# Kernel optimization log

Hardware: AMD Instinct MI355X
Metric: run time of the kernel (lower is better)

## Reference

```python
import jax, jax.numpy as jnp
import numpy as np

ALPHA = 0.05   # propalpha
GDEP = 2       # gcn_depth
DIL = 2        # new_dilation
KSET = (2, 3, 6, 7)

def _dconv(x, w, b, d):
    # Conv2d(c_in, c_out, (1, k), dilation=(1, d), padding='same'), NCHW layout
    k = w.shape[-1]
    tot = d * (k - 1)
    lo = tot // 2
    y = jax.lax.conv_general_dilated(x, w, (1, 1), ((0, 0), (lo, tot - lo)),
                                     rhs_dilation=(1, d),
                                     dimension_numbers=('NCHW', 'OIHW', 'NCHW'))
    return y + b[None, :, None, None]

def _inception(x, ws, bs):
    # 'same' padding keeps seq_len for every branch, so the tail-slice is a no-op
    return jnp.concatenate([_dconv(x, w, b, DIL) for w, b in zip(ws, bs)], axis=1)

def _gcn(Hf, Aoff, W, b, n):
    # PyG GCNConv with unit edge weights (no edge_weight passed) and remaining self-loops:
    # out = D^-1/2 (A_off + I_R)^T D^-1/2 (Hf @ W^T) + b, where only rows < n carry edges.
    XW = Hf @ W.T
    deg = jnp.ones((Hf.shape[0],), Hf.dtype).at[:n].add(jnp.sum(Aoff, axis=0))
    dis = jax.lax.rsqrt(deg)
    out = XW / deg[:, None]                                           # self-loop term
    out = out.at[:n].add(dis[:n, None] * (Aoff.T @ (dis[:n, None] * XW[:n])))
    return out + b[None, :]

def _mixprop(X, A, gws, gbs, mw, mb):
    B, C, n, L = X.shape
    # dense_to_sparse ignores weights here (none passed to GCNConv) -> binary adjacency;
    # add_remaining_self_loops replaces any diagonal entries, so zero the diagonal.
    Aoff = (A != 0).astype(X.dtype) * (1.0 - jnp.eye(n, dtype=X.dtype))
    H = X
    hops = [X]
    for i in range(GDEP):
        Hf = H.reshape(B * L, C * n)   # torch row-major reshape, replicated exactly
        H1 = _gcn(Hf, Aoff, gws[i], gbs[i], n)
        H = ALPHA * X + H1.reshape(B, C, n, L)
        hops.append(H)
    Hc = jnp.concatenate(hops, axis=1)  # (B, (GDEP+1)*C, n, L)
    return jnp.einsum('bixl,oi->boxl', Hc, mw) + mb[None, :, None, None]

def _layernorm(x, w, b, idx, eps=1e-5):
    # F.layer_norm over all of x.shape[1:] with node-indexed affine params
    mu = jnp.mean(x, axis=(1, 2, 3), keepdims=True)
    var = jnp.var(x, axis=(1, 2, 3), keepdims=True)
    xh = (x - mu) * jax.lax.rsqrt(var + eps)
    return xh * w[:, idx, :][None] + b[:, idx, :][None]

def _forward(x, x_skip, A, idx, fws, fbs, gws, gbs, skip_w, skip_b,
             mp1_gw, mp1_gb, mp1_mw, mp1_mb, mp2_gw, mp2_gb, mp2_mw, mp2_mb,
             ln_w, ln_b):
    x_res = x
    xf = jnp.tanh(_inception(x, fws, fbs))
    xg = jax.nn.sigmoid(_inception(x, gws, gbs))
    x = xf * xg  # gated dilated temporal conv (dropout is an eval-mode no-op)
    x_skip = jnp.einsum('bixl,oi->boxl', x, skip_w) + skip_b[None, :, None, None] + x_skip
    x = (_mixprop(x, A, mp1_gw, mp1_gb, mp1_mw, mp1_mb)
         + _mixprop(x.swapaxes(0, 0), A.T, mp2_gw, mp2_gb, mp2_mw, mp2_mb))
    x = x + x_res[..., -x.shape[3]:]
    x = _layernorm(x, ln_w, ln_b, idx)
    return x, x_skip

def setup_inputs():
    key = jax.random.key(0)
    ks = jax.random.split(key, 32)
    B, C, N, L, SKIP = 16, 32, 128, 128, 64
    F = C * N
    co = C // len(KSET)
    d = {}
    d['x'] = jax.random.normal(ks[0], (B, C, N, L), jnp.float32)
    d['x_skip'] = jax.random.normal(ks[1], (B, SKIP, N, L), jnp.float32)
    d['A'] = jax.random.uniform(ks[2], (N, N), jnp.float32)
    d['idx'] = jnp.arange(N, dtype=jnp.int32)
    i = 3
    for pre in ('f', 'g'):
        for k in KSET:
            d[pre + 'w' + str(k)] = jax.random.normal(ks[i], (co, C, 1, k), jnp.float32) * float(1.0 / np.sqrt(C * k))
            d[pre + 'b' + str(k)] = jax.random.uniform(ks[i + 1], (co,), jnp.float32)
            i += 2
    d['skip_w'] = jax.random.normal(ks[i], (SKIP, C), jnp.float32) * float(1.0 / np.sqrt(C)); i += 1
    d['skip_b'] = jax.random.uniform(ks[i], (SKIP,), jnp.float32); i += 1
    for mp in ('mp1', 'mp2'):
        d[mp + '_gw'] = jax.random.normal(ks[i], (GDEP, F, F), jnp.float32) * float(1.0 / np.sqrt(F)); i += 1
        d[mp + '_gb'] = jnp.zeros((GDEP, F), jnp.float32)
        d[mp + '_mw'] = jax.random.normal(ks[i], (C, (GDEP + 1) * C), jnp.float32) * float(1.0 / np.sqrt((GDEP + 1) * C)); i += 1
        d[mp + '_mb'] = jax.random.uniform(ks[i], (C,), jnp.float32); i += 1
    d['ln_w'] = jnp.ones((C, N, L), jnp.float32)
    d['ln_b'] = jnp.zeros((C, N, L), jnp.float32)
    return d

def reference(x, x_skip, A, idx, fw2, fb2, fw3, fb3, fw6, fb6, fw7, fb7,
              gw2, gb2, gw3, gb3, gw6, gb6, gw7, gb7, skip_w, skip_b,
              mp1_gw, mp1_gb, mp1_mw, mp1_mb, mp2_gw, mp2_gb, mp2_mw, mp2_mb,
              ln_w, ln_b):
    return _forward(x, x_skip, A, idx,
                    [fw2, fw3, fw6, fw7], [fb2, fb3, fb6, fb7],
                    [gw2, gw3, gw6, gw7], [gb2, gb3, gb6, gb7],
                    skip_w, skip_b, mp1_gw, mp1_gb, mp1_mw, mp1_mb,
                    mp2_gw, mp2_gb, mp2_mw, mp2_mb, ln_w, ln_b)
```

## Files before the change

### kernel.cpp

```cpp
#include <hip/hip_runtime.h>
#include <stdint.h>

typedef unsigned short u16;
typedef unsigned int   u32;
typedef __attribute__((ext_vector_type(4))) float f32x4;
typedef __attribute__((ext_vector_type(8))) short bf16x8;

__device__ __forceinline__ u16 f2bf(float f) {
    u32 i = __float_as_uint(f);
    u32 r = (i + 0x7fffu + ((i >> 16) & 1u)) >> 16;
    return (u16)r;
}
__device__ __forceinline__ float bf2f(u16 u) {
    return __uint_as_float(((u32)u) << 16);
}
__device__ __forceinline__ u32 cvt2bf(float a, float b) {
    u32 r;
    asm("v_cvt_pk_bf16_f32 %0, %1, %2" : "=v"(r) : "v"(a), "v"(b));
    return r;
}

#define GLOAD16(g, l) __builtin_amdgcn_global_load_lds( \
    (const __attribute__((address_space(1))) void*)(g), \
    (__attribute__((address_space(3))) void*)(l), 16, 0, 0)

__global__ void k_prep(const float* __restrict__ A, float* dis1, float* inv1,
                       float* dis2, float* inv2)
{
    int r = threadIdx.x;
    if (r >= 128) return;
    int cc = 0, cr = 0;
    for (int j = 0; j < 128; ++j) {
        if (j == r) continue;
        if (A[(j << 7) + r] != 0.f) cc++;
        if (A[(r << 7) + j] != 0.f) cr++;
    }
    float d1 = 1.f + (float)cc, d2 = 1.f + (float)cr;
    dis1[r] = rsqrtf(d1); inv1[r] = 1.f / d1;
    dis2[r] = rsqrtf(d2); inv2[r] = 1.f / d2;
}

__global__ __launch_bounds__(256)
void k_wcvt2(const float* __restrict__ W0, const float* __restrict__ W1,
             u16* __restrict__ Wb0, u16* __restrict__ Wb1)
{
    int half = blockIdx.x >> 13;
    const float* W = half ? W1 : W0;
    u16* Wb = half ? Wb1 : Wb0;
    size_t e = ((size_t)(blockIdx.x & 8191) * 256 + threadIdx.x) * 8;
    f32x4 a = *(const f32x4*)(W + e);
    f32x4 b = *(const f32x4*)(W + e + 4);
    uint4 r;
    r.x = cvt2bf(a[0], a[1]); r.y = cvt2bf(a[2], a[3]);
    r.z = cvt2bf(b[0], b[1]); r.w = cvt2bf(b[2], b[3]);
    *(uint4*)(Wb + e) = r;
}

__global__ __launch_bounds__(256, 2)
void k_gemm2g(const u16* __restrict__ A0, const u16* __restrict__ A1,
              const u16* __restrict__ B0, const u16* __restrict__ B1,
              const u16* __restrict__ Gres,
              const float* __restrict__ gb0, const float* __restrict__ gb1,
              u16* __restrict__ Ha, u16* __restrict__ Hb,
              float* __restrict__ XW0a, float* __restrict__ XW0b)
{
    __shared__ alignas(16) u16 As[128 * 32];
    __shared__ alignas(16) u16 Bs[128 * 32];
    const int K = 4096;
    const int tid  = threadIdx.x;
    const int lane = tid & 63;
    const int w    = tid >> 6;

    int bid = (blockIdx.z * gridDim.y + blockIdx.y) * gridDim.x + blockIdx.x;
    int swz = (bid & 7) * 128 + (bid >> 3);
    int z   = swz >> 9;
    int rem = swz & 511;
    const int bm = (rem >> 5) * 128, bn = (rem & 31) * 128;
    const int wm = (w >> 1) * 64,    wn = (w & 1) * 64;

    const u16* A = z ? A1 : A0;
    const u16* B = z ? B1 : B0;

    const int srow = tid >> 2, scol = (tid & 3) * 8;
    const u16* ag = A + (size_t)(bm + srow) * K + scol;
    const u16* bg = B + (size_t)(bn + srow) * K + scol;
    u16* asl = As + tid * 8;
    u16* bsl = Bs + tid * 8;
    const size_t rstep = (size_t)64 * K;

    f32x4 acc[4][4] = {};
    const int lr = lane & 15, lkb = (lane >> 4) * 8;

    for (int k0 = 0; k0 < K; k0 += 32) {
        GLOAD16(ag + k0,         asl);
        GLOAD16(ag + k0 + rstep, asl + 2048);
        GLOAD16(bg + k0,         bsl);
        GLOAD16(bg + k0 + rstep, bsl + 2048);
        __syncthreads();
        bf16x8 af[4], bfv[4];
        #pragma unroll
        for (int i = 0; i < 4; ++i) {
            af[i]  = *(const bf16x8*)(As + (wm + i * 16 + lr) * 32 + lkb);
            bfv[i] = *(const bf16x8*)(Bs + (wn + i * 16 + lr) * 32 + lkb);
        }
        #pragma unroll
        for (int i = 0; i < 4; ++i)
            #pragma unroll
            for (int j = 0; j < 4; ++j)
                acc[i][j] = __builtin_amdgcn_mfma_f32_16x16x32_bf16(af[i], bfv[j], acc[i][j], 0, 0, 0);
        __syncthreads();
    }

    const int orow = (lane >> 4) * 4, ocol = lane & 15;
    const float* gbv = z ? gb1 : gb0;
    u16* H = z ? Hb : Ha;

    #pragma unroll
    for (int j = 0; j < 4; ++j) {
        const int o = bn + wn + j * 16 + ocol;
        const float gbo = gbv[o];
        #pragma unroll
        for (int i = 0; i < 4; ++i) {
            const int rbase = bm + wm + i * 16 + orow;
            #pragma unroll
            for (int v = 0; v < 4; ++v) {
                const size_t e = (size_t)(rbase + v) * 4096 + o;
                float g = bf2f(Gres[e]);
                H[e] = f2bf(__fmaf_rn(0.05f, g, acc[i][j][v] + gbo));
            }
        }
    }
    if (bm == 0) {
        float* XW0 = z ? XW0b : XW0a;
        #pragma unroll
        for (int i = 0; i < 4; ++i) {
            #pragma unroll
            for (int j = 0; j < 4; ++j) {
                float* cp = XW0 + (size_t)(wm + i * 16 + orow) * 4096 + (bn + wn + j * 16 + ocol);
                #pragma unroll
                for (int v = 0; v < 4; ++v)
                    cp[(size_t)v * 4096] = acc[i][j][v];
            }
        }
    }
}

__global__ __launch_bounds__(256)
void k_gcnfix(const float* __restrict__ XW0a, const float* __restrict__ XW0b,
              const u16* __restrict__ G, const float* __restrict__ Af,
              const float* __restrict__ dis1, const float* __restrict__ inv1,
              const float* __restrict__ dis2, const float* __restrict__ inv2,
              const float* __restrict__ gb0, const float* __restrict__ gb1,
              u16* __restrict__ Ha, u16* __restrict__ Hb)
{
    const int prob = blockIdx.x >> 9;
    const int rem  = blockIdx.x & 511;
    const int t4 = rem * 256 + threadIdx.x;
    const int r = t4 >> 10, og = (t4 & 1023) << 2;
    const float* XW0 = prob ? XW0b : XW0a;
    const float* dis = prob ? dis2 : dis1;
    const float* inv = prob ? inv2 : inv1;
    const float* gb  = prob ? gb1  : gb0;
    u16* H = prob ? Hb : Ha;

    const size_t e = ((size_t)r << 12) + og;
    f32x4 xw = *(const f32x4*)(XW0 + e);
    f32x4 s = {0.f, 0.f, 0.f, 0.f};
    for (int j = 0; j < 128; ++j) {
        float av = prob ? Af[(r << 7) + j] : Af[(j << 7) + r];
        float wv = ((av != 0.f) && (j != r)) ? dis[j] : 0.f;
        f32x4 xv = *(const f32x4*)(XW0 + ((size_t)j << 12) + og);
        #pragma unroll
        for (int q = 0; q < 4; ++q) s[q] = __fmaf_rn(wv, xv[q], s[q]);
    }
    const float iv = inv[r], dr = dis[r];
    f32x4 gb4 = *(const f32x4*)(gb + og);
    uint2 gv = *(const uint2*)(G + e);
    float g0 = __uint_as_float(gv.x << 16), g1 = __uint_as_float(gv.x & 0xffff0000u);
    float g2 = __uint_as_float(gv.y << 16), g3 = __uint_as_float(gv.y & 0xffff0000u);
    float y0 = __fmaf_rn(0.05f, g0, __fmaf_rn(dr, s[0], xw[0] * iv) + gb4[0]);
    float y1 = __fmaf_rn(0.05f, g1, __fmaf_rn(dr, s[1], xw[1] * iv) + gb4[1]);
    float y2 = __fmaf_rn(0.05f, g2, __fmaf_rn(dr, s[2], xw[2] * iv) + gb4[2]);
    float y3 = __fmaf_rn(0.05f, g3, __fmaf_rn(dr, s[3], xw[3] * iv) + gb4[3]);
    uint2 rr;
    rr.x = cvt2bf(y0, y1);
    rr.y = cvt2bf(y2, y3);
    *(uint2*)(H + e) = rr;
}

__device__ __forceinline__ constexpr int wbase_of(int k) {
    return k == 2 ? 0 : k == 3 ? 520 : k == 6 ? 1296 : 2840;
}
__device__ __forceinline__ constexpr int ob_of(int k) {
    return k == 2 ? 0 : k == 3 ? 8 : k == 6 ? 16 : 24;
}

template<int K_>
__device__ __forceinline__ void conv_phase(const float* __restrict__ xsb,
                                           const float* __restrict__ wfp,
                                           const float* __restrict__ wgp,
                                           float fb, float gb,
                                           u16* __restrict__ Gp)
{
    float accf[8], accg[8];
    #pragma unroll
    for (int i = 0; i < 8; ++i) { accf[i] = fb; accg[i] = gb; }
    for (int c = 0; c < 32; ++c) {
        float xw[24];
        const float* xr = xsb + c * 144;
        #pragma unroll
        for (int q = 0; q < 6; ++q) {
            f32x4 v = *(const f32x4*)(xr + q * 4);
            xw[q * 4 + 0] = v[0]; xw[q * 4 + 1] = v[1];
            xw[q * 4 + 2] = v[2]; xw[q * 4 + 3] = v[3];
        }
        float wfj[K_], wgj[K_];
        const float* wfc = wfp + c * K_;
        const float* wgc = wgp + c * K_;
        #pragma unroll
        for (int j = 0; j < K_; ++j) { wfj[j] = wfc[j]; wgj[j] = wgc[j]; }
        #pragma unroll
        for (int li = 0; li < 8; ++li) {
            #pragma unroll
            for (int j = 0; j < K_; ++j) {
                float xv = xw[li + 8 - (K_ - 1) + 2 * j];
                accf[li] = __fmaf_rn(xv, wfj[j], accf[li]);
                accg[li] = __fmaf_rn(xv, wgj[j], accg[li]);
            }
        }
    }
    u16 o8[8];
    #pragma unroll
    for (int i = 0; i < 8; ++i) {
        float e2 = __expf(2.f * accf[i]);
        float th = 1.f - __fdividef(2.f, e2 + 1.f);
        float sg = __fdividef(1.f, 1.f + __expf(-accg[i]));
        o8[i] = f2bf(th * sg);
    }
    uint4 u;
    u.x = o8[0] | ((u32)o8[1] << 16); u.y = o8[2] | ((u32)o8[3] << 16);
    u.z = o8[4] | ((u32)o8[5] << 16); u.w = o8[6] | ((u32)o8[7] << 16);
    *(uint4*)Gp = u;
}

template<int KA, int KB>
__device__ __forceinline__ void wave_pair(const float* __restrict__ xs,
                                          const float* __restrict__ wfl,
                                          const float* __restrict__ wgl,
                                          const float* __restrict__ fbl,
                                          const float* __restrict__ gbl,
                                          int oo, int lL, int b, int n,
                                          u16* __restrict__ G)
{
    {
        constexpr int BS = wbase_of(KA), ST = 32 * KA + 1, OB = ob_of(KA);
        const int o = OB + oo, l0 = lL * 8;
        conv_phase<KA>(xs + l0, wfl + BS + oo * ST, wgl + BS + oo * ST,
                       fbl[o], gbl[o],
                       G + (((size_t)(b * 32 + o) * 128 + n) * 128 + l0));
    }
    {
        constexpr int BS = wbase_of(KB), ST = 32 * KB + 1, OB = ob_of(KB);
        const int o = OB + oo, l0 = 64 + lL * 8;
        conv_phase<KB>(xs + l0, wfl + BS + oo * ST, wgl + BS + oo * ST,
                       fbl[o], gbl[o],
                       G + (((size_t)(b * 32 + o) * 128 + n) * 128 + l0));
    }
}

__global__ __launch_bounds__(256)
void k_incep(const float* __restrict__ x,
             const float* __restrict__ fw2p, const float* __restrict__ fw3p,
             const float* __restrict__ fw6p, const float* __restrict__ fw7p,
             const float* __restrict__ fb2p, const float* __restrict__ fb3p,
             const float* __restrict__ fb6p, const float* __restrict__ fb7p,
             const float* __restrict__ gw2p, const float* __restrict__ gw3p,
             const float* __restrict__ gw6p, const float* __restrict__ gw7p,
             const float* __restrict__ gb2p, const float* __restrict__ gb3p,
             const float* __restrict__ gb6p, const float* __restrict__ gb7p,
             u16* __restrict__ G)
{
    __shared__ alignas(16) float xs[32 * 144];
    __shared__ float wfl[4640], wgl[4640];
    __shared__ float fbl[32], gbl[32];
    const int tid = threadIdx.x;
    const int b = blockIdx.x >> 7, n = blockIdx.x & 127;

    for (int i = tid; i < 32 * 144; i += 256) xs[i] = 0.f;
    for (int g = tid; g < 4608; g += 256) {
        int rel, k, woff;
        const float *pf, *pg;
        if (g < 512)       { rel = g;        k = 2; woff = 0;    pf = fw2p; pg = gw2p; }
        else if (g < 1280) { rel = g - 512;  k = 3; woff = 520;  pf = fw3p; pg = gw3p; }
        else if (g < 2816) { rel = g - 1280; k = 6; woff = 1296; pf = fw6p; pg = gw6p; }
        else               { rel = g - 2816; k = 7; woff = 2840; pf = fw7p; pg = gw7p; }
        int ck = 32 * k;
        int oo = rel / ck, rem = rel % ck;
        int dst = woff + oo * (ck + 1) + rem;
        wfl[dst] = pf[rel];
        wgl[dst] = pg[rel];
    }
    if (tid < 32) {
        int br = tid >> 3, oo = tid & 7;
        const float* pf = br == 0 ? fb2p : br == 1 ? fb3p : br == 2 ? fb6p : fb7p;
        const float* pg = br == 0 ? gb2p : br == 1 ? gb3p : br == 2 ? gb6p : gb7p;
        fbl[tid] = pf[oo]; gbl[tid] = pg[oo];
    }
    __syncthreads();
    const float* xb = x + (size_t)b * 524288 + n * 128;
    for (int p = 0; p < 4; ++p) {
        int chunk = p * 256 + tid;
        int c = chunk >> 5, l4 = (chunk & 31) * 4;
        *(f32x4*)&xs[c * 144 + 8 + l4] = *(const f32x4*)(xb + (size_t)c * 16384 + l4);
    }
    __syncthreads();

    const int w = tid >> 6, lane = tid & 63;
    const int oo = lane >> 3, lL = lane & 7;
    switch (w) {
        case 0:  wave_pair<2, 7>(xs, wfl, wgl, fbl, gbl, oo, lL, b, n, G); break;
        case 1:  wave_pair<7, 2>(xs, wfl, wgl, fbl, gbl, oo, lL, b, n, G); break;
        case 2:  wave_pair<3, 6>(xs, wfl, wgl, fbl, gbl, oo, lL, b, n, G); break;
        default: wave_pair<6, 3>(xs, wfl, wgl, fbl, gbl, oo, lL, b, n, G); break;
    }
}

__global__ __launch_bounds__(256)
void k_skip(const u16* __restrict__ G, const float* __restrict__ xskip,
            const float* __restrict__ sw, const float* __restrict__ sb,
            float* __restrict__ outp)
{
    __shared__ alignas(16) u16 Gs[4096];
    __shared__ float swl[64 * 33];
    __shared__ float sbl[64];
    const int tid = threadIdx.x;
    const int b = blockIdx.x >> 7, n = blockIdx.x & 127;
    const u16* gb_ = G + (size_t)b * 524288 + n * 128;
    for (int p = 0; p < 2; ++p) {
        int chunk = p * 256 + tid, c = chunk >> 4, l8 = (chunk & 15) * 8;
        *(uint4*)&Gs[c * 128 + l8] = *(const uint4*)(gb_ + (size_t)c * 16384 + l8);
    }
    for (int i = tid; i < 2048; i += 256) swl[(i >> 5) * 33 + (i & 31)] = sw[i];
    if (tid < 64) sbl[tid] = sb[tid];
    __syncthreads();
    const int sg = (tid & 15) * 4, l0 = (tid >> 4) * 8;
    float acc[4][8];
    #pragma unroll
    for (int si = 0; si < 4; ++si) {
        float bv = sbl[sg + si];
        #pragma unroll
        for (int li = 0; li < 8; ++li) acc[si][li] = bv;
    }
    for (int c = 0; c < 32; ++c) {
        uint4 gv = *(const uint4*)&Gs[c * 128 + l0];
        float g[8];
        g[0] = __uint_as_float(gv.x << 16); g[1] = __uint_as_float(gv.x & 0xffff0000u);
        g[2] = __uint_as_float(gv.y << 16); g[3] = __uint_as_float(gv.y & 0xffff0000u);
        g[4] = __uint_as_float(gv.z << 16); g[5] = __uint_as_float(gv.z & 0xffff0000u);
        g[6] = __uint_as_float(gv.w << 16); g[7] = __uint_as_float(gv.w & 0xffff0000u);
        #pragma unroll
        for (int si = 0; si < 4; ++si) {
            float wv = swl[(sg + si) * 33 + c];
            #pragma unroll
            for (int li = 0; li < 8; ++li) acc[si][li] = __fmaf_rn(g[li], wv, acc[si][li]);
        }
    }
    #pragma unroll
    for (int si = 0; si < 4; ++si) {
        size_t e = ((size_t)(b * 64 + sg + si) * 128 + n) * 128 + l0;
        f32x4 x0 = *(const f32x4*)(xskip + e);
        f32x4 x1 = *(const f32x4*)(xskip + e + 4);
        f32x4 r0, r1;
        r0[0] = acc[si][0] + x0[0]; r0[1] = acc[si][1] + x0[1];
        r0[2] = acc[si][2] + x0[2]; r0[3] = acc[si][3] + x0[3];
        r1[0] = acc[si][4] + x1[0]; r1[1] = acc[si][5] + x1[1];
        r1[2] = acc[si][6] + x1[2]; r1[3] = acc[si][7] + x1[3];
        *(f32x4*)(outp + e)     = r0;
        *(f32x4*)(outp + e + 4) = r1;
    }
}

__global__ __launch_bounds__(256)
void k_mix2ln(const u16* __restrict__ G,
              const u16* __restrict__ H1, const u16* __restrict__ H2,
              const u16* __restrict__ H1b, const u16* __restrict__ H2b,
              const float* __restrict__ mw1, const float* __restrict__ mb1,
              const float* __restrict__ mw2, const float* __restrict__ mb2,
              const float* __restrict__ x,
              float* __restrict__ Y, float* __restrict__ partial)
{
    __shared__ alignas(16) u16 Gs[4096], H1s[4096], H2s[4096], H1bs[4096], H2bs[4096];
    __shared__ float wSg[32 * 33], wS11[32 * 33], wS12[32 * 33], wS21[32 * 33], wS22[32 * 33];
    __shared__ float mbl[32];
    const int tid = threadIdx.x;
    const int b = blockIdx.x >> 7, xn = blockIdx.x & 127;
    size_t base = (size_t)b * 524288 + xn * 128;
    for (int p = 0; p < 2; ++p) {
        int chunk = p * 256 + tid, c = chunk >> 4, l8 = (chunk & 15) * 8;
        size_t src = base + (size_t)c * 16384 + l8;
        *(uint4*)&Gs[c * 128 + l8]   = *(const uint4*)(G + src);
        *(uint4*)&H1s[c * 128 + l8]  = *(const uint4*)(H1 + src);
        *(uint4*)&H2s[c * 128 + l8]  = *(const uint4*)(H2 + src);
        *(uint4*)&H1bs[c * 128 + l8] = *(const uint4*)(H1b + src);
        *(uint4*)&H2bs[c * 128 + l8] = *(const uint4*)(H2b + src);
    }
    for (int i = tid; i < 1024; i += 256) {
        int o = i >> 5, c = i & 31;
        int d = o * 33 + c;
        wSg[d]  = mw1[o * 96 + c] + mw2[o * 96 + c];
        wS11[d] = mw1[o * 96 + 32 + c];
        wS12[d] = mw1[o * 96 + 64 + c];
        wS21[d] = mw2[o * 96 + 32 + c];
        wS22[d] = mw2[o * 96 + 64 + c];
    }
    if (tid < 32) mbl[tid] = mb1[tid] + mb2[tid];
    __syncthreads();
    const int og = (tid & 7) * 4, l0 = (tid >> 3) * 4;
    float acc[4][4];
    #pragma unroll
    for (int oi = 0; oi < 4; ++oi) {
        float bv = mbl[og + oi];
        acc[oi][0] = bv; acc[oi][1] = bv; acc[oi][2] = bv; acc[oi][3] = bv;
    }
    for (int c = 0; c < 32; ++c) {
        uint2 ga = *(const uint2*)&Gs[c * 128 + l0];
        uint2 h1 = *(const uint2*)&H1s[c * 128 + l0];
        uint2 h2 = *(const uint2*)&H2s[c * 128 + l0];
        uint2 j1 = *(const uint2*)&H1bs[c * 128 + l0];
        uint2 j2 = *(const uint2*)&H2bs[c * 128 + l0];
        float gv[4], v1[4], v2[4], u1[4], u2[4];
        gv[0] = __uint_as_float(ga.x << 16); gv[1] = __uint_as_float(ga.x & 0xffff0000u);
        gv[2] = __uint_as_float(ga.y << 16); gv[3] = __uint_as_float(ga.y & 0xffff0000u);
        v1[0] = __uint_as_float(h1.x << 16); v1[1] = __uint_as_float(h1.x & 0xffff0000u);
        v1[2] = __uint_as_float(h1.y << 16); v1[3] = __uint_as_float(h1.y & 0xffff0000u);
        v2[0] = __uint_as_float(h2.x << 16); v2[1] = __uint_as_float(h2.x & 0xffff0000u);
        v2[2] = __uint_as_float(h2.y << 16); v2[3] = __uint_as_float(h2.y & 0xffff0000u);
        u1[0] = __uint_as_float(j1.x << 16); u1[1] = __uint_as_float(j1.x & 0xffff0000u);
        u1[2] = __uint_as_float(j1.y << 16); u1[3] = __uint_as_float(j1.y & 0xffff0000u);
        u2[0] = __uint_as_float(j2.x << 16); u2[1] = __uint_as_float(j2.x & 0xffff0000u);
        u2[2] = __uint_as_float(j2.y << 16); u2[3] = __uint_as_float(j2.y & 0xffff0000u);
        #pragma unroll
        for (int oi = 0; oi < 4; ++oi) {
            int d = (og + oi) * 33 + c;
            float a0 = wSg[d], a1 = wS11[d], a2 = wS12[d], a3 = wS21[d], a4 = wS22[d];
            #pragma unroll
            for (int li = 0; li < 4; ++li)
                acc[oi][li] += gv[li] * a0 + v1[li] * a1 + v2[li] * a2
                             + u1[li] * a3 + u2[li] * a4;
        }
    }
    float s = 0.f, ss = 0.f;
    #pragma unroll
    for (int oi = 0; oi < 4; ++oi) {
        size_t e = ((size_t)(b * 32 + og + oi) * 128 + xn) * 128 + l0;
        f32x4 xv = *(const f32x4*)(x + e);
        f32x4 yv;
        #pragma unroll
        for (int li = 0; li < 4; ++li) {
            float y = acc[oi][li] + xv[li];
            yv[li] = y;
            s += y; ss += y * y;
        }
        *(f32x4*)(Y + e) = yv;
    }
    #pragma unroll
    for (int o = 32; o > 0; o >>= 1) {
        s  += __shfl_down(s,  o, 64);
        ss += __shfl_down(ss, o, 64);
    }
    __shared__ float sred[8];
    int w = tid >> 6;
    if ((tid & 63) == 0) { sred[w * 2] = s; sred[w * 2 + 1] = ss; }
    __syncthreads();
    if (tid == 0) {
        partial[blockIdx.x * 2]     = sred[0] + sred[2] + sred[4] + sred[6];
        partial[blockIdx.x * 2 + 1] = sred[1] + sred[3] + sred[5] + sred[7];
    }
}

__global__ __launch_bounds__(256)
void k_lnnorm(const float* __restrict__ Y,
              const float* __restrict__ partial, const int* __restrict__ idxp,
              const float* __restrict__ lnw, const float* __restrict__ lnb,
              float* __restrict__ outx)
{
    const int tid = threadIdx.x;
    const int b = blockIdx.x >> 7, chunk = blockIdx.x & 127;
    float s = 0.f, ss = 0.f;
    if (tid < 128) {
        s  = partial[(b * 128 + tid) * 2];
        ss = partial[(b * 128 + tid) * 2 + 1];
    }
    #pragma unroll
    for (int o = 32; o > 0; o >>= 1) {
        s  += __shfl_down(s,  o, 64);
        ss += __shfl_down(ss, o, 64);
    }
    __shared__ float sred[4];
    __shared__ float mv[2];
    if ((tid & 63) == 0 && tid < 128) { sred[(tid >> 6) * 2] = s; sred[(tid >> 6) * 2 + 1] = ss; }
    __syncthreads();
    if (tid == 0) {
        float S = sred[0] + sred[2], SS = sred[1] + sred[3];
        float mean = S * (1.f / 524288.f);
        float var = SS * (1.f / 524288.f) - mean * mean;
        mv[0] = mean; mv[1] = rsqrtf(var + 1e-5f);
    }
    __syncthreads();
    const float mean = mv[0], rstd = mv[1];
    #pragma unroll
    for (int q = 0; q < 4; ++q) {
        int ib = chunk * 4096 + q * 1024 + tid * 4;
        size_t e = (size_t)b * 524288 + ib;
        f32x4 yv = *(const f32x4*)(Y + e);
        int c = ib >> 14, xn = (ib >> 7) & 127, l = ib & 127;
        int ix = idxp[xn];
        size_t we = ((size_t)c * 128 + ix) * 128 + l;
        f32x4 wv = *(const f32x4*)(lnw + we);
        f32x4 bv = *(const f32x4*)(lnb + we);
        f32x4 r;
        #pragma unroll
        for (int j = 0; j < 4; ++j)
            r[j] = (yv[j] - mean) * rstd * wv[j] + bv[j];
        *(f32x4*)(outx + e) = r;
    }
}

extern "C" void kernel_launch(void* const* d_in, const int* in_sizes, int n_in,
                              void* d_out, int out_size, void* d_ws, size_t ws_size,
                              hipStream_t stream)
{
    (void)in_sizes; (void)n_in; (void)out_size; (void)ws_size;
    const float* x      = (const float*)d_in[0];
    const float* xskip  = (const float*)d_in[1];
    const float* A      = (const float*)d_in[2];
    const int*   idxp   = (const int*)d_in[3];
    const float* fw2p = (const float*)d_in[4];  const float* fb2p = (const float*)d_in[5];
    const float* fw3p = (const float*)d_in[6];  const float* fb3p = (const float*)d_in[7];
    const float* fw6p = (const float*)d_in[8];  const float* fb6p = (const float*)d_in[9];
    const float* fw7p = (const float*)d_in[10]; const float* fb7p = (const float*)d_in[11];
    const float* gw2p = (const float*)d_in[12]; const float* gb2p = (const float*)d_in[13];
    const float* gw3p = (const float*)d_in[14]; const float* gb3p = (const float*)d_in[15];
    const float* gw6p = (const float*)d_in[16]; const float* gb6p = (const float*)d_in[17];
    const float* gw7p = (const float*)d_in[18]; const float* gb7p = (const float*)d_in[19];
    const float* sw   = (const float*)d_in[20]; const float* sb   = (const float*)d_in[21];
    const float* mp1_gw = (const float*)d_in[22]; const float* mp1_gb = (const float*)d_in[23];
    const float* mp1_mw = (const float*)d_in[24]; const float* mp1_mb = (const float*)d_in[25];
    const float* mp2_gw = (const float*)d_in[26]; const float* mp2_gb = (const float*)d_in[27];
    const float* mp2_mw = (const float*)d_in[28]; const float* mp2_mb = (const float*)d_in[29];
    const float* lnw = (const float*)d_in[30]; const float* lnb = (const float*)d_in[31];

    char* wsb = (char*)d_ws;
    float* out_x  = (float*)d_out;
    float* out_sk = out_x + 8388608;

    const size_t MB16 = 16777216, MB33 = 33554432;
    u16*   G    = (u16*)(wsb);
    u16*   H1   = (u16*)(wsb + MB16);
    u16*   H1b  = (u16*)(wsb + 2 * MB16);
    u16*   H2   = (u16*)(wsb + 3 * MB16);
    u16*   H2b  = (u16*)(wsb + 4 * MB16);
    u16*   Wb0  = (u16*)(wsb + 5 * MB16);
    u16*   Wb1  = (u16*)(wsb + 5 * MB16 + MB33);
    float* Yb   = (float*)Wb0;
    float* XW0a = (float*)(wsb + 5 * MB16 + 2 * MB33);
    float* XW0b = (float*)(wsb + 5 * MB16 + 2 * MB33 + 2097152);
    float* part = (float*)(wsb + 5 * MB16 + 2 * MB33 + 4194304);
    float* dd   = (float*)(wsb + 5 * MB16 + 2 * MB33 + 4194304 + 16384);
    float *dis1 = dd, *inv1 = dd + 128, *dis2 = dd + 256, *inv2 = dd + 384;

    k_prep<<<1, 128, 0, stream>>>(A, dis1, inv1, dis2, inv2);
    k_incep<<<2048, 256, 0, stream>>>(x, fw2p, fw3p, fw6p, fw7p, fb2p, fb3p, fb6p, fb7p,
                                      gw2p, gw3p, gw6p, gw7p, gb2p, gb3p, gb6p, gb7p, G);
    k_skip<<<2048, 256, 0, stream>>>(G, xskip, sw, sb, out_sk);

    dim3 gg2(32, 16, 2);
    k_wcvt2<<<16384, 256, 0, stream>>>(mp1_gw, mp2_gw, Wb0, Wb1);
    k_gemm2g<<<gg2, 256, 0, stream>>>(G, G, Wb0, Wb1, G, mp1_gb, mp2_gb,
                                      H1, H1b, XW0a, XW0b);
    k_gcnfix<<<1024, 256, 0, stream>>>(XW0a, XW0b, G, A, dis1, inv1, dis2, inv2,
                                       mp1_gb, mp2_gb, H1, H1b);
    k_wcvt2<<<16384, 256, 0, stream>>>(mp1_gw + MB16, mp2_gw + MB16, Wb0, Wb1);
    k_gemm2g<<<gg2, 256, 0, stream>>>(H1, H1b, Wb0, Wb1, G, mp1_gb + 4096, mp2_gb + 4096,
                                      H2, H2b, XW0a, XW0b);
    k_gcnfix<<<1024, 256, 0, stream>>>(XW0a, XW0b, G, A, dis1, inv1, dis2, inv2,
                                       mp1_gb + 4096, mp2_gb + 4096, H2, H2b);
    k_mix2ln<<<2048, 256, 0, stream>>>(G, H1, H2, H1b, H2b, mp1_mw, mp1_mb,
                                       mp2_mw, mp2_mb, x, Yb, part);
    k_lnnorm<<<2048, 256, 0, stream>>>(Yb, part, idxp, lnw, lnb, out_x);
}
```

Baseline: 738.6 us.

## Restructure GCN GEMM into 256x256 tiles with 4-stage LDS prefetch pipeline

The bf16 GEMM for the GCN hops moves from 128x128 tiles with 256 threads and a single-buffered synchronous LDS loop to 256x256 tiles with 512 threads. A four-deep ring of LDS buffers is filled by async global-to-LDS loads issued three steps ahead, gated by explicit vmcnt waits. An XOR swizzle on the LDS layout avoids bank conflicts. The goal is to hide global latency and raise data reuse per tile, at the cost of 128KB LDS, one block per CU and only 256 blocks in the grid.

```diff
diff --git a/kernel.cpp b/kernel.cpp
--- a/kernel.cpp
+++ b/kernel.cpp
@@ -56,7 +56,7 @@
     *(uint4*)(Wb + e) = r;
 }
 
-__global__ __launch_bounds__(256, 2)
+__global__ __launch_bounds__(512, 1)
 void k_gemm2g(const u16* __restrict__ A0, const u16* __restrict__ A1,
               const u16* __restrict__ B0, const u16* __restrict__ B1,
               const u16* __restrict__ Gres,
@@ -64,52 +64,84 @@
               u16* __restrict__ Ha, u16* __restrict__ Hb,
               float* __restrict__ XW0a, float* __restrict__ XW0b)
 {
-    __shared__ alignas(16) u16 As[128 * 32];
-    __shared__ alignas(16) u16 Bs[128 * 32];
-    const int K = 4096;
+    __shared__ alignas(16) u16 LDS[65536];
+    const int NT = 128;
     const int tid  = threadIdx.x;
     const int lane = tid & 63;
-    const int w    = tid >> 6;
-
-    int bid = (blockIdx.z * gridDim.y + blockIdx.y) * gridDim.x + blockIdx.x;
-    int swz = (bid & 7) * 128 + (bid >> 3);
-    int z   = swz >> 9;
-    int rem = swz & 511;
-    const int bm = (rem >> 5) * 128, bn = (rem & 31) * 128;
-    const int wm = (w >> 1) * 64,    wn = (w & 1) * 64;
-
-    const u16* A = z ? A1 : A0;
-    const u16* B = z ? B1 : B0;
-
-    const int srow = tid >> 2, scol = (tid & 3) * 8;
-    const u16* ag = A + (size_t)(bm + srow) * K + scol;
-    const u16* bg = B + (size_t)(bn + srow) * K + scol;
-    u16* asl = As + tid * 8;
-    u16* bsl = Bs + tid * 8;
-    const size_t rstep = (size_t)64 * K;
-
-    f32x4 acc[4][4] = {};
-    const int lr = lane & 15, lkb = (lane >> 4) * 8;
-
-    for (int k0 = 0; k0 < K; k0 += 32) {
-        GLOAD16(ag + k0,         asl);
-        GLOAD16(ag + k0 + rstep, asl + 2048);
-        GLOAD16(bg + k0,         bsl);
-        GLOAD16(bg + k0 + rstep, bsl + 2048);
-        __syncthreads();
-        bf16x8 af[4], bfv[4];
-        #pragma unroll
-        for (int i = 0; i < 4; ++i) {
-            af[i]  = *(const bf16x8*)(As + (wm + i * 16 + lr) * 32 + lkb);
-            bfv[i] = *(const bf16x8*)(Bs + (wn + i * 16 + lr) * 32 + lkb);
-        }
-        #pragma unroll
-        for (int i = 0; i < 4; ++i)
+    const int wid  = tid >> 6;
+    const int wr = wid >> 2, wc = wid & 3;
+
+    const int bid = blockIdx.x;
+    const int swz = (bid & 7) * 32 + (bid >> 3);
+    const int z   = swz >> 7;
+    const int rem = swz & 127;
+    const int bm = (rem >> 4) * 256;
+    const int bn = (rem & 15) * 256;
+
+    const u16* Ap = (z ? A1 : A0) + (size_t)bm * 4096;
+    const u16* Bp = (z ? B1 : B0) + (size_t)bn * 4096;
+
+    int aoff[8];
+    #pragma unroll
+    for (int i = 0; i < 8; ++i) {
+        int ra = wr * 128 + i * 16 + (lane & 15);
+        int sp = (lane >> 4) ^ ((ra >> 1) & 3);
+        aoff[i] = ra * 32 + sp * 8;
+    }
+    int boff[4];
+    #pragma unroll
+    for (int j = 0; j < 4; ++j) {
+        int rb = wc * 64 + j * 16 + (lane & 15);
+        int sp = (lane >> 4) ^ ((rb >> 1) & 3);
+        boff[j] = rb * 32 + sp * 8;
+    }
+
+    f32x4 acc[8][4] = {};
+
+    auto stage = [&](int t) {
+        const int k0  = t << 5;
+        const int buf = (t & 3) << 14;
+        #pragma unroll
+        for (int h = 0; h < 2; ++h) {
+            const int ch = tid + h * 512;
+            const int r  = ch >> 2;
+            const int sl = (ch & 3) ^ ((r >> 1) & 3);
+            GLOAD16(Ap + (size_t)r * 4096 + k0 + sl * 8, LDS + buf + ch * 8);
+            GLOAD16(Bp + (size_t)r * 4096 + k0 + sl * 8, LDS + buf + 8192 + ch * 8);
+        }
+    };
+    auto compute = [&](int t) {
+        const u16* base = LDS + ((t & 3) << 14);
+        bf16x8 af[8], bv[4];
+        #pragma unroll
+        for (int i = 0; i < 8; ++i) af[i] = *(const bf16x8*)(base + aoff[i]);
+        #pragma unroll
+        for (int j = 0; j < 4; ++j) bv[j] = *(const bf16x8*)(base + 8192 + boff[j]);
+        #pragma unroll
+        for (int i = 0; i < 8; ++i)
             #pragma unroll
             for (int j = 0; j < 4; ++j)
-                acc[i][j] = __builtin_amdgcn_mfma_f32_16x16x32_bf16(af[i], bfv[j], acc[i][j], 0, 0, 0);
+                acc[i][j] = __builtin_amdgcn_mfma_f32_16x16x32_bf16(af[i], bv[j], acc[i][j], 0, 0, 0);
+    };
+
+    stage(0); stage(1); stage(2);
+    asm volatile("s_waitcnt vmcnt(8)" ::: "memory");
+    __syncthreads();
+
+    int t = 0;
+    for (; t < NT - 3; ++t) {
+        stage(t + 3);
+        compute(t);
+        asm volatile("s_waitcnt vmcnt(8)" ::: "memory");
         __syncthreads();
     }
+    compute(t);
+    asm volatile("s_waitcnt vmcnt(4)" ::: "memory");
+    __syncthreads(); ++t;
+    compute(t);
+    asm volatile("s_waitcnt vmcnt(0)" ::: "memory");
+    __syncthreads(); ++t;
+    compute(t);
 
     const int orow = (lane >> 4) * 4, ocol = lane & 15;
     const float* gbv = z ? gb1 : gb0;
@@ -117,11 +149,11 @@
 
     #pragma unroll
     for (int j = 0; j < 4; ++j) {
-        const int o = bn + wn + j * 16 + ocol;
+        const int o = bn + wc * 64 + j * 16 + ocol;
         const float gbo = gbv[o];
         #pragma unroll
-        for (int i = 0; i < 4; ++i) {
-            const int rbase = bm + wm + i * 16 + orow;
+        for (int i = 0; i < 8; ++i) {
+            const int rbase = bm + wr * 128 + i * 16 + orow;
             #pragma unroll
             for (int v = 0; v < 4; ++v) {
                 const size_t e = (size_t)(rbase + v) * 4096 + o;
@@ -130,13 +162,13 @@
             }
         }
     }
-    if (bm == 0) {
+    if (bm == 0 && wr == 0) {
         float* XW0 = z ? XW0b : XW0a;
         #pragma unroll
-        for (int i = 0; i < 4; ++i) {
+        for (int i = 0; i < 8; ++i) {
             #pragma unroll
             for (int j = 0; j < 4; ++j) {
-                float* cp = XW0 + (size_t)(wm + i * 16 + orow) * 4096 + (bn + wn + j * 16 + ocol);
+                float* cp = XW0 + (size_t)(i * 16 + orow) * 4096 + (bn + wc * 64 + j * 16 + ocol);
                 #pragma unroll
                 for (int v = 0; v < 4; ++v)
                     cp[(size_t)v * 4096] = acc[i][j][v];
@@ -574,14 +606,13 @@
                                       gw2p, gw3p, gw6p, gw7p, gb2p, gb3p, gb6p, gb7p, G);
     k_skip<<<2048, 256, 0, stream>>>(G, xskip, sw, sb, out_sk);
 
-    dim3 gg2(32, 16, 2);
     k_wcvt2<<<16384, 256, 0, stream>>>(mp1_gw, mp2_gw, Wb0, Wb1);
-    k_gemm2g<<<gg2, 256, 0, stream>>>(G, G, Wb0, Wb1, G, mp1_gb, mp2_gb,
+    k_gemm2g<<<256, 512, 0, stream>>>(G, G, Wb0, Wb1, G, mp1_gb, mp2_gb,
                                       H1, H1b, XW0a, XW0b);
     k_gcnfix<<<1024, 256, 0, stream>>>(XW0a, XW0b, G, A, dis1, inv1, dis2, inv2,
                                        mp1_gb, mp2_gb, H1, H1b);
     k_wcvt2<<<16384, 256, 0, stream>>>(mp1_gw + MB16, mp2_gw + MB16, Wb0, Wb1);
-    k_gemm2g<<<gg2, 256, 0, stream>>>(H1, H1b, Wb0, Wb1, G, mp1_gb + 4096, mp2_gb + 4096,
+    k_gemm2g<<<256, 512, 0, stream>>>(H1, H1b, Wb0, Wb1, G, mp1_gb + 4096, mp2_gb + 4096,
                                       H2, H2b, XW0a, XW0b);
     k_gcnfix<<<1024, 256, 0, stream>>>(XW0a, XW0b, G, A, dis1, inv1, dis2, inv2,
                                        mp1_gb + 4096, mp2_gb + 4096, H2, H2b);
```

After: 719.7 us. 1.03x faster.
